# Kernel tuning notes

Measured on AMD Instinct MI355X. Metric: run time of the kernel, lower is better.

Reference implementation:

```python
import jax, jax.numpy as jnp
import numpy as np

TAU = 1.0
BETA = 0.1
MIN_NORM = 1.0
B = 4194304


def setup_inputs() -> dict:
    key = jax.random.key(0)
    # positions spread over the four-well landscape (minima near (0.5+-1, 0.5+-1))
    batch = jax.random.normal(key, (B, 2), dtype=jnp.float32) * 1.5
    return {"batch": batch}


def reference(batch):
    batch = batch.reshape(-1, 2)
    u = batch[..., 0] - 0.5
    v = batch[..., 1] - 0.5

    # potential V4 = (u^2-1)^2 + (v^2-1)^2 + beta*u*v
    energy = (u * u - 1.0) ** 2 + (v * v - 1.0) ** 2 + BETA * u * v

    # analytic gradient, forces = -grad
    gx = 4.0 * u * (u * u - 1.0) + BETA * v
    gy = 4.0 * v * (v * v - 1.0) + BETA * u
    forces = -jnp.stack((gx, gy), axis=-1)  # (B, 2)

    # analytic Hessian (B, 2, 2)
    hxx = 12.0 * (u * u) - 4.0
    hyy = 12.0 * (v * v) - 4.0
    hxy = jnp.full_like(hxx, BETA)
    hessian = jnp.stack(
        (jnp.stack((hxx, hxy), axis=-1), jnp.stack((hxy, hyy), axis=-1)), axis=-2
    )

    # eigh: ascending eigenvalues, matching torch.linalg.eigh convention
    eigenvals, eigenvecs = jnp.linalg.eigh(hessian)
    smallest_eigvec = eigenvecs[..., :, 0]  # (B, 2)

    # GAD direction: reflect forces along smallest-eigenvalue eigenvector
    gad = -forces + 2.0 * jnp.sum(forces * smallest_eigvec, axis=-1, keepdims=True) * smallest_eigvec

    # norm_gad_outside_ts branch: normalize gad outside saddle region if small
    eigval_product = eigenvals[..., 0] * eigenvals[..., 1]
    gad_mag = jnp.linalg.norm(gad, axis=-1, keepdims=True)  # (B, 1)
    mask = (eigval_product > 0) & (gad_mag[..., 0] < MIN_NORM)
    gad = jnp.where(mask[..., None], gad / jnp.maximum(gad_mag, 1e-30), gad)

    energy_grad = gad / TAU
    return energy, forces, energy_grad, hessian, eigenvals[..., 0], eigenvals[..., 1]
```

## Files before the change

kernel.cpp:

```cpp
#include <hip/hip_runtime.h>


typedef float f2v __attribute__((ext_vector_type(2)));
typedef float f4v __attribute__((ext_vector_type(4)));

__global__ __launch_bounds__(256, 8) void fw_energy_gad_kernel(
    const f2v* __restrict__ in, float* __restrict__ out, int n) {
    int i = blockIdx.x * blockDim.x + threadIdx.x;
    if (i >= n) return;

    const float BETA = 0.1f;

    f2v p = in[i];
    float u = p.x - 0.5f;
    float v = p.y - 0.5f;
    float uu = u * u;
    float vv = v * v;
    float a = uu - 1.0f;
    float b = vv - 1.0f;

    float energy = a * a + b * b + BETA * u * v;

    float gx = 4.0f * u * a + BETA * v;
    float gy = 4.0f * v * b + BETA * u;
    float fx = -gx;
    float fy = -gy;

    float hxx = 12.0f * uu - 4.0f;
    float hyy = 12.0f * vv - 4.0f;

    float d = 0.5f * (hxx - hyy);
    float m = 0.5f * (hxx + hyy);
    float r = __builtin_amdgcn_sqrtf(d * d + BETA * BETA);
    float l0 = m - r;
    float l1 = m + r;

    bool pos = (d >= 0.0f);
    float wx = pos ? BETA : (d - r);
    float wy = pos ? -(d + r) : BETA;
    float n2 = wx * wx + wy * wy;

    float fd = fx * wx + fy * wy;
    float s = (2.0f * fd) * __builtin_amdgcn_rcpf(n2);
    float gadx = -fx + s * wx;
    float gady = -fy + s * wy;

    float prod = l0 * l1;
    float g2 = gadx * gadx + gady * gady;
    if (prod > 0.0f && g2 < 1.0f) {
        float inv = __builtin_amdgcn_rsqf(fmaxf(g2, 1e-60f));
        gadx *= inv;
        gady *= inv;
    }

    size_t N = (size_t)n;
    float* e_out  = out;
    f2v*   f_out  = (f2v*)(out + N);
    f2v*   g_out  = (f2v*)(out + 3 * N);
    f4v*   h_out  = (f4v*)(out + 5 * N);
    float* l0_out = out + 9 * N;
    float* l1_out = out + 10 * N;

    e_out[i] = energy;
    f2v fo; fo.x = fx; fo.y = fy;
    f_out[i] = fo;
    f2v go; go.x = gadx; go.y = gady;
    g_out[i] = go;
    f4v ho; ho.x = hxx; ho.y = BETA; ho.z = BETA; ho.w = hyy;
    h_out[i] = ho;
    l0_out[i] = l0;
    l1_out[i] = l1;
}

extern "C" void kernel_launch(void* const* d_in, const int* in_sizes, int n_in,
                              void* d_out, int out_size, void* d_ws, size_t ws_size,
                              hipStream_t stream) {
    const f2v* in = (const f2v*)d_in[0];
    float* out = (float*)d_out;
    int n = in_sizes[0] / 2;

    int block = 256;
    int grid = (n + block - 1) / block;
    fw_energy_gad_kernel<<<grid, block, 0, stream>>>(in, out, n);
}
```

Baseline: 198.2 us.

## Stage input tile in LDS, then compute and store per-thread in phases

```diff
diff --git a/kernel.cpp b/kernel.cpp
--- a/kernel.cpp
+++ b/kernel.cpp
@@ -4,56 +4,26 @@
 typedef float f2v __attribute__((ext_vector_type(2)));
 typedef float f4v __attribute__((ext_vector_type(4)));
 
-__global__ __launch_bounds__(256, 8) void fw_energy_gad_kernel(
+#define BLOCK 256
+#define PTS_PER_BLOCK 4096
+#define ITERS (PTS_PER_BLOCK / BLOCK)
+
+__global__ __launch_bounds__(BLOCK) void fw_phased_kernel(
     const f2v* __restrict__ in, float* __restrict__ out, int n) {
-    int i = blockIdx.x * blockDim.x + threadIdx.x;
-    if (i >= n) return;
+    __shared__ f2v smem[PTS_PER_BLOCK];
 
     const float BETA = 0.1f;
+    int t = threadIdx.x;
+    size_t N = (size_t)n;
+    size_t base = (size_t)blockIdx.x * PTS_PER_BLOCK;
 
-    f2v p = in[i];
-    float u = p.x - 0.5f;
-    float v = p.y - 0.5f;
-    float uu = u * u;
-    float vv = v * v;
-    float a = uu - 1.0f;
-    float b = vv - 1.0f;
+    #pragma unroll
+    for (int k = 0; k < ITERS; ++k) {
+        size_t idx = base + (size_t)(t + k * BLOCK);
+        if (idx < N) smem[t + k * BLOCK] = in[idx];
+    }
+    __syncthreads();
 
-    float energy = a * a + b * b + BETA * u * v;
-
-    float gx = 4.0f * u * a + BETA * v;
-    float gy = 4.0f * v * b + BETA * u;
-    float fx = -gx;
-    float fy = -gy;
-
-    float hxx = 12.0f * uu - 4.0f;
-    float hyy = 12.0f * vv - 4.0f;
-
-    float d = 0.5f * (hxx - hyy);
-    float m = 0.5f * (hxx + hyy);
-    float r = __builtin_amdgcn_sqrtf(d * d + BETA * BETA);
-    float l0 = m - r;
-    float l1 = m + r;
-
-    bool pos = (d >= 0.0f);
-    float wx = pos ? BETA : (d - r);
-    float wy = pos ? -(d + r) : BETA;
-    float n2 = wx * wx + wy * wy;
-
-    float fd = fx * wx + fy * wy;
-    float s = (2.0f * fd) * __builtin_amdgcn_rcpf(n2);
-    float gadx = -fx + s * wx;
-    float gady = -fy + s * wy;
-
-    float prod = l0 * l1;
-    float g2 = gadx * gadx + gady * gady;
-    if (prod > 0.0f && g2 < 1.0f) {
-        float inv = __builtin_amdgcn_rsqf(fmaxf(g2, 1e-60f));
-        gadx *= inv;
-        gady *= inv;
-    }
-
-    size_t N = (size_t)n;
     float* e_out  = out;
     f2v*   f_out  = (f2v*)(out + N);
     f2v*   g_out  = (f2v*)(out + 3 * N);
@@ -61,15 +31,65 @@
     float* l0_out = out + 9 * N;
     float* l1_out = out + 10 * N;
 
-    e_out[i] = energy;
-    f2v fo; fo.x = fx; fo.y = fy;
-    f_out[i] = fo;
-    f2v go; go.x = gadx; go.y = gady;
-    g_out[i] = go;
-    f4v ho; ho.x = hxx; ho.y = BETA; ho.z = BETA; ho.w = hyy;
-    h_out[i] = ho;
-    l0_out[i] = l0;
-    l1_out[i] = l1;
+    #pragma unroll 4
+    for (int k = 0; k < ITERS; ++k) {
+        int p = t + k * BLOCK;
+        size_t i = base + (size_t)p;
+        if (i < N) {
+            f2v pt = smem[p];
+
+            float u = pt.x - 0.5f;
+            float v = pt.y - 0.5f;
+            float uu = u * u;
+            float vv = v * v;
+            float a = uu - 1.0f;
+            float b = vv - 1.0f;
+
+            float energy = a * a + b * b + BETA * u * v;
+
+            float gx = 4.0f * u * a + BETA * v;
+            float gy = 4.0f * v * b + BETA * u;
+            float fx = -gx;
+            float fy = -gy;
+
+            float hxx = 12.0f * uu - 4.0f;
+            float hyy = 12.0f * vv - 4.0f;
+
+            float d = 0.5f * (hxx - hyy);
+            float m = 0.5f * (hxx + hyy);
+            float r = __builtin_amdgcn_sqrtf(d * d + BETA * BETA);
+            float l0 = m - r;
+            float l1 = m + r;
+
+            bool pos = (d >= 0.0f);
+            float wx = pos ? BETA : (d - r);
+            float wy = pos ? -(d + r) : BETA;
+            float n2 = wx * wx + wy * wy;
+
+            float fd = fx * wx + fy * wy;
+            float s = (2.0f * fd) * __builtin_amdgcn_rcpf(n2);
+            float gadx = -fx + s * wx;
+            float gady = -fy + s * wy;
+
+            float prod = l0 * l1;
+            float g2 = gadx * gadx + gady * gady;
+            if (prod > 0.0f && g2 < 1.0f) {
+                float inv = __builtin_amdgcn_rsqf(fmaxf(g2, 1e-60f));
+                gadx *= inv;
+                gady *= inv;
+            }
+
+            e_out[i] = energy;
+            f2v fo; fo.x = fx; fo.y = fy;
+            f_out[i] = fo;
+            f2v go; go.x = gadx; go.y = gady;
+            g_out[i] = go;
+            f4v ho; ho.x = hxx; ho.y = BETA; ho.z = BETA; ho.w = hyy;
+            h_out[i] = ho;
+            l0_out[i] = l0;
+            l1_out[i] = l1;
+        }
+    }
 }
 
 extern "C" void kernel_launch(void* const* d_in, const int* in_sizes, int n_in,
@@ -79,7 +99,7 @@
     float* out = (float*)d_out;
     int n = in_sizes[0] / 2;
 
-    int block = 256;
-    int grid = (n + block - 1) / block;
-    fw_energy_gad_kernel<<<grid, block, 0, stream>>>(in, out, n);
+    int grid = (n + PTS_PER_BLOCK - 1) / PTS_PER_BLOCK;
+    if (grid < 1) grid = 1;
+    fw_phased_kernel<<<grid, BLOCK, 0, stream>>>(in, out, n);
 }
```

Measured after the change: 201.6 us. Within noise of the previous version (+1.7%).
